# Kernel tuning notes

Measured on AMD Instinct MI355X. Metric: run time of the kernel, lower is better.

Reference implementation:

```python
import jax, jax.numpy as jnp
import numpy as np

N_BITS = 8
DEGREE = 8
F_IN = 1024
F_OUT = 1024
SEED = 69
B = 16
T = 4096


def _build_mixer_and_perm():
    # cyclic band mask: sum of identity rolled along rows by 1..degree-1
    eye = np.eye(F_OUT, F_IN, dtype=np.float32)
    cyclemask = np.zeros((F_OUT, F_IN), dtype=bool)
    for i in range(1, DEGREE):
        cyclemask |= np.roll(eye, i, axis=0).astype(bool)
    rng = np.random.RandomState(SEED)
    mixer = np.zeros((F_OUT, F_IN), dtype=np.float32)
    # LFSR.gen_fxp_shift(n_bits): low-bit fixed-point shift values (powers of two)
    nnz = int(cyclemask.sum())
    mixer[cyclemask] = (2.0 ** (-rng.randint(0, N_BITS, size=nnz))).astype(np.float32)
    permutation = rng.permutation(F_IN).astype(np.int32)
    return jnp.asarray(mixer), jnp.asarray(permutation)


def setup_inputs() -> dict:
    key = jax.random.key(0)
    x = jax.random.normal(key, (B, F_IN, T), dtype=jnp.float32)
    mixer, permutation = _build_mixer_and_perm()
    return {"x": x, "mixer": mixer, "permutation": permutation}


def reference(x, mixer, permutation):
    # gather-permute features, then banded (materialized-dense) mix
    xp = x[:, permutation, :]                     # [B, f_in, T]
    return jnp.einsum("oi,bit->bot", mixer, xp)   # [B, f_out, T]
```

## Files before the change

### kernel.cpp

```cpp
#include <hip/hip_runtime.h>


#define F_DIM 1024
#define T_DIM 4096
#define T4 (T_DIM / 4)
#define OCH 32
#define ROWS_PER_BLOCK 128

typedef float fvec4 __attribute__((ext_vector_type(4)));

__global__ __launch_bounds__(256, 4) void lowbit_mix_kernel(
    const float* __restrict__ x, const float* __restrict__ mixer,
    const int* __restrict__ perm, float* __restrict__ out)
{
    __shared__ float sCoef[ROWS_PER_BLOCK][8];
    __shared__ int   sPerm[136];

    const int tid  = threadIdx.x;
    const int lane = tid & 63;
    const int w    = tid >> 6;
    const int t4   = blockIdx.x * 64 + lane;
    const int block_o0 = blockIdx.y * ROWS_PER_BLOCK;
    const int b    = blockIdx.z;

#pragma unroll
    for (int idx = tid; idx < ROWS_PER_BLOCK * 8; idx += 256) {
        const int r = idx >> 3;
        const int d = (idx & 7) + 1;
        const int o = block_o0 + r;
        sCoef[r][d - 1] = mixer[(size_t)o * F_DIM + ((o - d) & (F_DIM - 1))];
    }
    if (tid < 136) {
        sPerm[tid] = perm[(block_o0 - 8 + tid) & (F_DIM - 1)];
    }
    __syncthreads();

    const fvec4* __restrict__ xb =
        reinterpret_cast<const fvec4*>(x) + (size_t)b * F_DIM * T4;
    fvec4* __restrict__ ob =
        reinterpret_cast<fvec4*>(out) + (size_t)b * F_DIM * T4;

    const int wbase = w * OCH;
    fvec4 win[7];
#pragma unroll
    for (int k = 0; k < 7; ++k) {
        win[k] = xb[(size_t)sPerm[wbase + 1 + k] * T4 + t4];
    }

#pragma unroll
    for (int oi = 0; oi < OCH; ++oi) {
        const int r = wbase + oi;
        const int o = block_o0 + r;

        fvec4 nxt;
        if (oi != OCH - 1) {
            nxt = xb[(size_t)sPerm[r + 8] * T4 + t4];
        }

        fvec4 acc = (fvec4)(0.f);
#pragma unroll
        for (int d = 7; d >= 1; --d) {
            const float c = sCoef[r][d - 1];
            acc += c * win[7 - d];
        }
        __builtin_nontemporal_store(acc, &ob[(size_t)o * T4 + t4]);

        if (oi != OCH - 1) {
#pragma unroll
            for (int k = 0; k < 6; ++k) win[k] = win[k + 1];
            win[6] = nxt;
        }
    }
}

extern "C" void kernel_launch(void* const* d_in, const int* in_sizes, int n_in,
                              void* d_out, int out_size, void* d_ws, size_t ws_size,
                              hipStream_t stream) {
    const float* x     = (const float*)d_in[0];
    const float* mixer = (const float*)d_in[1];
    const int*   perm  = (const int*)d_in[2];
    float*       out   = (float*)d_out;

    dim3 grid(T_DIM / 256,
              F_DIM / ROWS_PER_BLOCK,
              16);
    dim3 block(256);
    lowbit_mix_kernel<<<grid, block, 0, stream>>>(x, mixer, perm, out);
}
```

Baseline: 99.64 us.

## Pack band coefficients in prep kernel and broadcast via readlane instead of LDS

A small prep kernel now extracts the seven band coefficients per output row into a packed workspace array. The main kernel stops staging coefficients and permutation indices in shared memory and drops the __syncthreads. Each wave instead loads its own slice into registers and broadcasts values with readlane. The intent is to remove the strided mixer gathers, the LDS traffic and the block barrier, and to raise the occupancy hint to 6, at the cost of an extra kernel launch.

```diff
diff --git a/kernel.cpp b/kernel.cpp
--- a/kernel.cpp
+++ b/kernel.cpp
@@ -9,58 +9,60 @@
 
 typedef float fvec4 __attribute__((ext_vector_type(4)));
 
-__global__ __launch_bounds__(256, 4) void lowbit_mix_kernel(
-    const float* __restrict__ x, const float* __restrict__ mixer,
+__global__ __launch_bounds__(256) void prep_kernel(const float* __restrict__ mixer,
+                                                   float* __restrict__ coefPacked) {
+    const int o = blockIdx.x * 256 + threadIdx.x;
+#pragma unroll
+    for (int j = 0; j < 8; ++j) {
+        float c = 0.f;
+        if (j < 7) c = mixer[(size_t)o * F_DIM + ((o - (j + 1)) & (F_DIM - 1))];
+        coefPacked[o * 8 + j] = c;
+    }
+}
+
+__global__ __launch_bounds__(256, 6) void lowbit_mix_kernel(
+    const float* __restrict__ x, const float* __restrict__ coefPacked,
     const int* __restrict__ perm, float* __restrict__ out)
 {
-    __shared__ float sCoef[ROWS_PER_BLOCK][8];
-    __shared__ int   sPerm[136];
-
     const int tid  = threadIdx.x;
     const int lane = tid & 63;
     const int w    = tid >> 6;
     const int t4   = blockIdx.x * 64 + lane;
-    const int block_o0 = blockIdx.y * ROWS_PER_BLOCK;
+    const int o0   = blockIdx.y * ROWS_PER_BLOCK + w * OCH;
     const int b    = blockIdx.z;
 
-#pragma unroll
-    for (int idx = tid; idx < ROWS_PER_BLOCK * 8; idx += 256) {
-        const int r = idx >> 3;
-        const int d = (idx & 7) + 1;
-        const int o = block_o0 + r;
-        sCoef[r][d - 1] = mixer[(size_t)o * F_DIM + ((o - d) & (F_DIM - 1))];
-    }
-    if (tid < 136) {
-        sPerm[tid] = perm[(block_o0 - 8 + tid) & (F_DIM - 1)];
-    }
-    __syncthreads();
+    const int vperm = perm[(o0 - 8 + lane) & (F_DIM - 1)];
+    const fvec4 vc = *reinterpret_cast<const fvec4*>(&coefPacked[(size_t)o0 * 8 + lane * 4]);
 
     const fvec4* __restrict__ xb =
         reinterpret_cast<const fvec4*>(x) + (size_t)b * F_DIM * T4;
     fvec4* __restrict__ ob =
         reinterpret_cast<fvec4*>(out) + (size_t)b * F_DIM * T4;
 
-    const int wbase = w * OCH;
     fvec4 win[7];
 #pragma unroll
     for (int k = 0; k < 7; ++k) {
-        win[k] = xb[(size_t)sPerm[wbase + 1 + k] * T4 + t4];
+        const int pi = __builtin_amdgcn_readlane(vperm, 1 + k);
+        win[k] = xb[(size_t)pi * T4 + t4];
     }
 
 #pragma unroll
     for (int oi = 0; oi < OCH; ++oi) {
-        const int r = wbase + oi;
-        const int o = block_o0 + r;
+        const int o = o0 + oi;
 
         fvec4 nxt;
         if (oi != OCH - 1) {
-            nxt = xb[(size_t)sPerm[r + 8] * T4 + t4];
+            const int pi = __builtin_amdgcn_readlane(vperm, 8 + oi);
+            nxt = xb[(size_t)pi * T4 + t4];
         }
 
         fvec4 acc = (fvec4)(0.f);
 #pragma unroll
         for (int d = 7; d >= 1; --d) {
-            const float c = sCoef[r][d - 1];
+            const int e    = (d - 1);
+            const int ln   = oi * 2 + (e >> 2);
+            const float c  = __uint_as_float(
+                (unsigned)__builtin_amdgcn_readlane(__float_as_uint(vc[e & 3]), ln));
             acc += c * win[7 - d];
         }
         __builtin_nontemporal_store(acc, &ob[(size_t)o * T4 + t4]);
@@ -80,10 +82,13 @@
     const float* mixer = (const float*)d_in[1];
     const int*   perm  = (const int*)d_in[2];
     float*       out   = (float*)d_out;
+    float*       coefPacked = (float*)d_ws;
+
+    prep_kernel<<<dim3(4), dim3(256), 0, stream>>>(mixer, coefPacked);
 
     dim3 grid(T_DIM / 256,
               F_DIM / ROWS_PER_BLOCK,
               16);
     dim3 block(256);
-    lowbit_mix_kernel<<<grid, block, 0, stream>>>(x, mixer, perm, out);
+    lowbit_mix_kernel<<<grid, block, 0, stream>>>(x, coefPacked, perm, out);
 }
```

New measurement: 102.5 us. 2.9% more time.
